# Optimization experiments

Measured on AMD Instinct MI355X. Metric: run time of the kernel, lower is better.

The kernel has to match this reference:

```python
import jax, jax.numpy as jnp
import numpy as np

D_MODEL = 2048
D_INNER = 4096      # expand * d_model
HEADDIM = 64
NHEADS = 64         # d_inner // headdim
D_STATE = 128
NGROUPS = 1
D_CONV = 4
CHUNK = 128
EPS = 1e-5
BATCH = 2
SEQLEN = 4096
D_CONV_CH = D_INNER + 2 * NGROUPS * D_STATE            # 4352
D_IN_PROJ = 2 * D_INNER + 2 * NGROUPS * D_STATE + NHEADS  # 8512


def setup_inputs() -> dict:
    ks = jax.random.split(jax.random.key(0), 9)
    u = jax.random.normal(ks[0], (BATCH, SEQLEN, D_MODEL), jnp.float32)
    W_in = jax.random.normal(ks[1], (D_MODEL, D_IN_PROJ), jnp.float32) * 0.02
    conv_w = jax.random.normal(ks[2], (D_CONV_CH, D_CONV), jnp.float32) * 0.2
    conv_b = jax.random.normal(ks[3], (D_CONV_CH,), jnp.float32) * 0.02
    dt_bias = jax.random.normal(ks[4], (NHEADS,), jnp.float32) * 0.1
    A_log = jax.random.normal(ks[5], (NHEADS,), jnp.float32) * 0.1
    D = jnp.ones((NHEADS,), jnp.float32)
    norm_w = jnp.ones((D_INNER,), jnp.float32)
    W_out = jax.random.normal(ks[8], (D_INNER, D_MODEL), jnp.float32) * 0.02
    return dict(u=u, W_in=W_in, conv_w=conv_w, conv_b=conv_b, dt_bias=dt_bias,
                A_log=A_log, D=D, norm_w=norm_w, W_out=W_out)


def _mamba2_forward(u, W_in, conv_w, conv_b, dt_bias, A_log, D, norm_w, W_out):
    b, L, _ = u.shape
    zxbcdt = u @ W_in                                       # (b, L, 8512)
    z = zxbcdt[..., :D_INNER]
    xBC = zxbcdt[..., D_INNER:D_INNER + D_CONV_CH]
    dt = zxbcdt[..., D_INNER + D_CONV_CH:]                  # (b, L, h)

    # causal depthwise conv1d (padding = d_conv-1, truncated to L) + SiLU
    padded = jnp.pad(xBC, ((0, 0), (D_CONV - 1, 0), (0, 0)))
    xBC_conv = conv_b + sum(padded[:, k:k + L, :] * conv_w[:, k] for k in range(D_CONV))
    xBC_act = jax.nn.silu(xBC_conv)

    x = xBC_act[..., :D_INNER].reshape(b, L, NHEADS, HEADDIM)
    Bm = xBC_act[..., D_INNER:D_INNER + NGROUPS * D_STATE].reshape(b, L, NGROUPS, D_STATE)
    Cm = xBC_act[..., D_INNER + NGROUPS * D_STATE:].reshape(b, L, NGROUPS, D_STATE)
    rep = NHEADS // NGROUPS
    Bh = jnp.repeat(Bm, rep, axis=2)                        # (b, L, h, n)
    Ch = jnp.repeat(Cm, rep, axis=2)

    A = -jnp.exp(A_log)                                     # (h,), negative
    dtf = jax.nn.softplus(dt + dt_bias)                     # (b, L, h)

    # ---- chunked SSD (structured state-space duality) scan ----
    nc = L // CHUNK
    xc = x.reshape(b, nc, CHUNK, NHEADS, HEADDIM)
    Bc = Bh.reshape(b, nc, CHUNK, NHEADS, D_STATE)
    Cc = Ch.reshape(b, nc, CHUNK, NHEADS, D_STATE)
    dtc = dtf.reshape(b, nc, CHUNK, NHEADS)
    cum = jnp.cumsum(dtc * A, axis=2)                       # (b, nc, cs, h), decreasing

    # intra-chunk causal decay matrix L_ij = exp(cum_i - cum_j), i >= j
    idx = jnp.arange(CHUNK)
    mask = (idx[:, None] >= idx[None, :])[None, None, :, :, None]
    seg = cum[:, :, :, None, :] - cum[:, :, None, :, :]     # (b, nc, i, j, h)
    decay = jnp.exp(jnp.where(mask, seg, -jnp.inf))
    CB = jnp.einsum('bcihn,bcjhn->bcijh', Cc, Bc)
    Y_diag = jnp.einsum('bcijh,bcjh,bcjhp->bcihp', CB * decay, dtc, xc)

    # per-chunk final states: sum_j exp(cum_last - cum_j) * dt_j * B_j (x) x_j
    decay_last = jnp.exp(cum[:, :, -1:, :] - cum)           # (b, nc, cs, h)
    states = jnp.einsum('bclh,bclhn,bclhp->bchpn', decay_last * dtc, Bc, xc)

    # inter-chunk recurrence: carry_{c+1} = exp(sum dA_c) * carry_c + states_c
    Atot = jnp.exp(cum[:, :, -1, :])                        # (b, nc, h)
    def step(carry, inp):
        a, s = inp
        return a[..., None, None] * carry + s, carry
    init = jnp.zeros((b, NHEADS, HEADDIM, D_STATE), jnp.float32)
    _, prev = jax.lax.scan(step, init, (jnp.moveaxis(Atot, 1, 0), jnp.moveaxis(states, 1, 0)))
    prev = jnp.moveaxis(prev, 0, 1)                         # (b, nc, h, p, n) state entering each chunk

    Y_off = jnp.einsum('bclhn,bclh,bchpn->bclhp', Cc, jnp.exp(cum), prev)

    y = (Y_diag + Y_off).reshape(b, L, NHEADS, HEADDIM) + D[:, None] * x
    y = y.reshape(b, L, D_INNER)

    # gated RMSNorm: rmsnorm(y * silu(z)) * norm_w
    t = y * jax.nn.silu(z)
    t = t * jax.lax.rsqrt(jnp.mean(t * t, axis=-1, keepdims=True) + EPS) * norm_w
    return t @ W_out


def reference(u, W_in, conv_w, conv_b, dt_bias, A_log, D, norm_w, W_out):
    return _mamba2_forward(u, W_in, conv_w, conv_b, dt_bias, A_log, D, norm_w, W_out)
```

## Files before the change

### kernel.cpp

```cpp
#include <hip/hip_runtime.h>

#define BATCH 2
#define SEQLEN 4096
#define DM 2048
#define DIP 8512
#define DIPP 8576
#define DI 4096
#define DCC 4352
#define NH 64
#define HD 64
#define DSZ 128
#define CHK 128
#define NC 32
#define NBL (BATCH*SEQLEN)
#define LDP 136

typedef __attribute__((ext_vector_type(4))) float f32x4;
typedef __attribute__((ext_vector_type(8))) __bf16 bf16x8;
typedef __attribute__((ext_vector_type(8))) unsigned short us8;
typedef __attribute__((ext_vector_type(4))) unsigned short us4;

__device__ inline float bf2f(unsigned short u){ union{unsigned int i; float f;} v; v.i=((unsigned)u)<<16; return v.f; }
__device__ inline unsigned short f2bf(float f){ union{float f; unsigned int i;} v; v.f=f; unsigned r=(v.i + 0x7FFFu + ((v.i>>16)&1u))>>16; return (unsigned short)r; }

#define GLOAD_LDS16(gp, lp) __builtin_amdgcn_global_load_lds( \
    (const __attribute__((address_space(1))) void*)(gp), \
    (__attribute__((address_space(3))) void*)(lp), 16, 0, 0)

__global__ void beacon_kernel(float* __restrict__ out, float v)
{
    if (blockIdx.x == 0 && threadIdx.x == 0) out[0] = v;
}

__global__ void cast_bf16_kernel(const float* __restrict__ src, unsigned short* __restrict__ dst, size_t n)
{
    size_t stride = (size_t)gridDim.x * blockDim.x * 8;
    for (size_t i = ((size_t)blockIdx.x*blockDim.x + threadIdx.x)*8; i < n; i += stride) {
        float4 a = *(const float4*)&src[i];
        float4 b = *(const float4*)&src[i+4];
        us8 o;
        o[0]=f2bf(a.x); o[1]=f2bf(a.y); o[2]=f2bf(a.z); o[3]=f2bf(a.w);
        o[4]=f2bf(b.x); o[5]=f2bf(b.y); o[6]=f2bf(b.z); o[7]=f2bf(b.w);
        *(us8*)&dst[i] = o;
    }
}

__global__ __launch_bounds__(256) void transpose_cast_kernel(
    const float* __restrict__ in, unsigned short* __restrict__ out, int R, int C)
{
    __shared__ float tile[32][33];
    const int c0 = blockIdx.x*32, r0 = blockIdx.y*32;
    const int tx = threadIdx.x & 31, ty = threadIdx.x >> 5;
    #pragma unroll
    for (int i = 0; i < 4; i++) {
        const int r = r0 + ty + i*8;
        const int c = c0 + tx;
        tile[ty+i*8][tx] = (c < C) ? in[(size_t)r*C + c] : 0.f;
    }
    __syncthreads();
    #pragma unroll
    for (int i = 0; i < 4; i++) {
        const int cc = c0 + ty + i*8;
        const int rr = r0 + tx;
        out[(size_t)cc*R + rr] = f2bf(tile[tx][ty+i*8]);
    }
}

template<int EPI>
__global__ __launch_bounds__(512, 1) void gemm256(
    const unsigned short* __restrict__ A, const unsigned short* __restrict__ Bt,
    float* __restrict__ C, int K, int ldc, int Nmax,
    unsigned short* __restrict__ zbf, unsigned short* __restrict__ xbcbf,
    float* __restrict__ dtf, const float* __restrict__ dt_bias)
{
    __shared__ unsigned short L[65536];
    const int m0 = blockIdx.x * 256;
    const int n0 = blockIdx.y * 256;
    const int tid = threadIdx.x;
    const int lane = tid & 63;
    const int wid  = tid >> 6;
    const int wm = wid >> 2, wn = wid & 3;
    const int lr  = lane & 15;
    const int lkg = (lane >> 4) * 8;
    const int srow = (wid << 4) + (lane >> 3);
    const int scol = ((lane & 7) ^ (lane >> 3)) << 3;
    const int cs0 = lkg ^ ((lr & 7) << 3);
    const int cs1 = cs0 ^ 32;
    const int nt = K >> 6;

    f32x4 acc[8][4];
    #pragma unroll
    for (int i=0;i<8;i++)
        #pragma unroll
        for (int j=0;j<4;j++) acc[i][j] = f32x4{0.f,0.f,0.f,0.f};

    auto stA = [&](int buf, int t, int h) {
        const unsigned short* g = A + (size_t)(m0 + h*128 + srow)*K + t*64 + scol;
        GLOAD_LDS16(g,               &L[buf*32768 + h*8192 + wid*1024]);
        GLOAD_LDS16(g + (size_t)8*K, &L[buf*32768 + h*8192 + wid*1024 + 512]);
    };
    auto stB = [&](int buf, int t, int h) {
        const int rr = n0 + h*128 + srow;
        const int r0 = (rr     > Nmax) ? Nmax : rr;
        const int r1 = (rr + 8 > Nmax) ? Nmax : rr + 8;
        GLOAD_LDS16(Bt + (size_t)r0*K + t*64 + scol, &L[buf*32768 + 16384 + h*8192 + wid*1024]);
        GLOAD_LDS16(Bt + (size_t)r1*K + t*64 + scol, &L[buf*32768 + 16384 + h*8192 + wid*1024 + 512]);
    };
    auto rdA = [&](int buf, int mq, int s, int ks) {
        const int rl = mq*32 + s*16 + lr;
        return *(const bf16x8*)&L[buf*32768 + wm*8192 + rl*64 + (ks ? cs1 : cs0)];
    };
    auto rdB = [&](int buf, int nf, int ks) {
        const int rl = (wn & 1)*64 + nf*16 + lr;
        return *(const bf16x8*)&L[buf*32768 + 16384 + (wn >> 1)*8192 + rl*64 + (ks ? cs1 : cs0)];
    };

    bf16x8 bfr[4][2];
#define PH(BUF, MQ, LOADB, ...) do { \
    bf16x8 af[2][2]; \
    af[0][0]=rdA(BUF,MQ,0,0); af[0][1]=rdA(BUF,MQ,0,1); \
    af[1][0]=rdA(BUF,MQ,1,0); af[1][1]=rdA(BUF,MQ,1,1); \
    if (LOADB) { \
        _Pragma("unroll") \
        for (int nf=0;nf<4;nf++){ bfr[nf][0]=rdB(BUF,nf,0); bfr[nf][1]=rdB(BUF,nf,1);} } \
    __VA_ARGS__; \
    if (LOADB) asm volatile("s_waitcnt lgkmcnt(8)" ::: "memory"); \
    asm volatile("s_barrier" ::: "memory"); \
    __builtin_amdgcn_s_setprio(1); \
    _Pragma("unroll") \
    for (int s=0;s<2;s++) { \
        _Pragma("unroll") \
        for (int nf=0;nf<4;nf++) { \
            acc[(MQ)*2+s][nf] = __builtin_amdgcn_mfma_f32_16x16x32_bf16(af[s][0], bfr[nf][0], acc[(MQ)*2+s][nf], 0,0,0); \
            acc[(MQ)*2+s][nf] = __builtin_amdgcn_mfma_f32_16x16x32_bf16(af[s][1], bfr[nf][1], acc[(MQ)*2+s][nf], 0,0,0); } } \
    __builtin_amdgcn_s_setprio(0); \
    asm volatile("s_barrier" ::: "memory"); \
} while(0)

    stA(0, 0, 0); stA(0, 0, 1); stB(0, 0, 0); stB(0, 0, 1);
    stB(1, 1, 0); stB(1, 1, 1);
    asm volatile("s_waitcnt vmcnt(4)" ::: "memory");
    asm volatile("s_barrier" ::: "memory");

    #pragma unroll 1
    for (int t = 0; t < nt; t += 2) {
        const int tp2 = (t + 2 < nt) ? t + 2 : nt - 1;
        const int tp3 = (t + 3 < nt) ? t + 3 : nt - 1;
        PH(0, 0, true,  stA(1, t+1, 0));
        PH(0, 1, false, stA(1, t+1, 1); stB(0, tp2, 0));
        PH(0, 2, false, stB(0, tp2, 1));
        PH(0, 3, false, asm volatile("s_waitcnt vmcnt(4)" ::: "memory"));
        PH(1, 0, true,  stA(0, tp2, 0));
        PH(1, 1, false, stA(0, tp2, 1); stB(1, tp3, 0));
        PH(1, 2, false, stB(1, tp3, 1));
        PH(1, 3, false, asm volatile("s_waitcnt vmcnt(4)" ::: "memory"));
    }
#undef PH

    const int cr = (lane >> 4) * 4;
    const int cc = lane & 15;
    #pragma unroll
    for (int i=0;i<8;i++) {
        #pragma unroll
        for (int j=0;j<4;j++) {
            const int row = m0 + wm*128 + i*16 + cr;
            const int col = n0 + wn*64 + j*16 + cc;
            #pragma unroll
            for (int r=0;r<4;r++) {
                const float val = acc[i][j][r];
                const int rr = row + r;
                if (EPI == 0) {
                    C[(size_t)rr*ldc + col] = val;
                } else {
                    if (col < DI) {
                        zbf[(size_t)rr*DI + col] = f2bf(val);
                    } else if (col < DI + DCC) {
                        xbcbf[(size_t)rr*DCC + (col - DI)] = f2bf(val);
                    } else if (col < DI + DCC + NH) {
                        const int hh = col - (DI + DCC);
                        const float x = val + dt_bias[hh];
                        dtf[(size_t)rr*NH + hh] = (x > 20.f) ? x : log1pf(__expf(x));
                    }
                }
            }
        }
    }
}

__global__ __launch_bounds__(256) void conv_x_kernel(
    const unsigned short* __restrict__ xbc,
    const float* __restrict__ cw, const float* __restrict__ cb,
    unsigned short* __restrict__ xT,
    unsigned short* __restrict__ bcbf)
{
    __shared__ float raw[67][68];
    __shared__ unsigned short ot[64][72];
    const int lt = blockIdx.x;
    const int h  = blockIdx.y;
    const int b  = lt >> 6;
    const int l0 = (lt & 63) * 64;
    const int t = threadIdx.x;

    if (h >= 64) {
        const int g4 = h - 64;
        #pragma unroll
        for (int j = 0; j < 2; j++) {
            const int u = t + j*256;
            const int l = u >> 3, pg = (u & 7)*8;
            const int ch0 = DI + g4*64 + pg;
            const int row = b*SEQLEN + l0 + l;
            float a[8];
            #pragma unroll
            for (int e=0;e<8;e++) a[e] = cb[ch0+e];
            #pragma unroll
            for (int k = 0; k < 4; k++) {
                if (l0 + l + k >= 3) {
                    us8 v = *(const us8*)&xbc[(size_t)(row + k - 3)*DCC + ch0];
                    #pragma unroll
                    for (int e=0;e<8;e++) a[e] += bf2f(v[e]) * cw[(ch0+e)*4 + k];
                }
            }
            us8 o;
            #pragma unroll
            for (int e=0;e<8;e++){ const float s = a[e]/(1.f+__expf(-a[e])); o[e]=f2bf(s); }
            *(us8*)&bcbf[(size_t)row*256 + g4*64 + pg] = o;
        }
        return;
    }

    for (int i = t; i < 536; i += 256) {
        const int li = i >> 3, cg = (i & 7) * 8;
        const int l = l0 - 3 + li;
        us8 v;
        #pragma unroll
        for (int e = 0; e < 8; e++) v[e] = 0;
        if (l >= 0) v = *(const us8*)&xbc[(size_t)(b*SEQLEN + l)*DCC + h*64 + cg];
        #pragma unroll
        for (int e = 0; e < 8; e++) raw[li][cg+e] = bf2f(v[e]);
    }
    __syncthreads();
    #pragma unroll
    for (int j = 0; j < 16; j++) {
        const int i = t + j*256;
        const int l = i >> 6, p = i & 63;
        const int ch = h*64 + p;
        float a = cb[ch];
        #pragma unroll
        for (int k = 0; k < 4; k++) a += raw[l + k][p] * cw[ch*4 + k];
        a = a / (1.f + __expf(-a));
        ot[l][p] = f2bf(a);
    }
    __syncthreads();
    for (int i = t; i < 512; i += 256) {
        const int p = i >> 3, lg = (i & 7) * 8;
        us8 o;
        #pragma unroll
        for (int e = 0; e < 8; e++) o[e] = ot[lg + e][p];
        *(us8*)&xT[(size_t)((b*NH + h)*HD + p)*SEQLEN + l0 + lg] = o;
    }
}

__global__ void cum_kernel(const float* __restrict__ dtf, const float* __restrict__ A_log,
                           float* __restrict__ cum)
{
    const int idx = blockIdx.x*blockDim.x + threadIdx.x;
    if (idx >= BATCH*NC*NH) return;
    const int h = idx & 63;
    const int bc = idx >> 6;
    const float A = -__expf(A_log[h]);
    float c = 0.f;
    const float* src = dtf + (size_t)bc*CHK*NH + h;
    float* dst = cum + (size_t)bc*CHK*NH + h;
    for (int i = 0; i < CHK; i++) { c += src[i*NH]*A; dst[i*NH] = c; }
}

__global__ __launch_bounds__(256, 3) void ssm_passS(
    const unsigned short* __restrict__ bcbf,
    const unsigned short* __restrict__ xT,
    const float* __restrict__ cumg,
    const float* __restrict__ dtfg,
    unsigned short* __restrict__ states)
{
    __shared__ unsigned short BT[128*LDP];
    __shared__ float w_s[128];

    const int blk = blockIdx.x;
    const int h = blk & 63;
    const int bc = blk >> 6;
    const int r0 = bc * CHK;
    const int t = threadIdx.x;
    const int lane = t & 63;
    const int wid = t >> 6;

    if (t < 128) {
        const float cl = cumg[(size_t)(r0+127)*NH + h];
        const float ci = cumg[(size_t)(r0+t)*NH + h];
        const float dt = dtfg[(size_t)(r0+t)*NH + h];
        w_s[t] = __expf(cl - ci) * dt;
    }
    for (int i = t; i < 2048; i += 256) {
        const int l = i >> 4, cg = (i & 15)*8;
        us8 v = *(const us8*)(bcbf + (size_t)(r0+l)*256 + cg);
        #pragma unroll
        for (int e = 0; e < 8; e++) BT[(cg+e)*LDP + l] = v[e];
    }
    __syncthreads();

    const int lr = lane & 15;
    const int lkg = (lane >> 4)*8;
    const int wr = wid >> 1, wc = wid & 1;
    const int b = bc >> 5;
    const int li = (bc & 31) * CHK;
    const unsigned short* xb = xT + (size_t)((b*NH + h)*HD)*SEQLEN + li;

    f32x4 acc[2][4];
    #pragma unroll
    for (int i=0;i<2;i++)
        #pragma unroll
        for (int j=0;j<4;j++) acc[i][j] = f32x4{0.f,0.f,0.f,0.f};
    #pragma unroll
    for (int k = 0; k < 4; k++) {
        bf16x8 a[2], bfr[4];
        #pragma unroll
        for (int i=0;i<2;i++) {
            us8 xv = *(const us8*)(xb + (size_t)(wr*32 + i*16 + lr)*SEQLEN + k*32 + lkg);
            us8 aw;
            #pragma unroll
            for (int e=0;e<8;e++) aw[e] = f2bf(bf2f(xv[e]) * w_s[k*32 + lkg + e]);
            a[i] = __builtin_bit_cast(bf16x8, aw);
        }
        #pragma unroll
        for (int j=0;j<4;j++) bfr[j] = *(const bf16x8*)&BT[(wc*64 + j*16 + lr)*LDP + k*32 + lkg];
        #pragma unroll
        for (int i=0;i<2;i++)
            #pragma unroll
            for (int j=0;j<4;j++)
                acc[i][j] = __builtin_amdgcn_mfma_f32_16x16x32_bf16(a[i], bfr[j], acc[i][j], 0,0,0);
    }
    unsigned short* sb = states + (size_t)blk * (HD*DSZ);
    const int cr = (lane >> 4)*4, cc = lane & 15;
    #pragma unroll
    for (int i=0;i<2;i++) {
        #pragma unroll
        for (int j=0;j<4;j++) {
            const int nn = wc*64 + j*16 + cc;
            #pragma unroll
            for (int r=0;r<4;r++) {
                const int pp = wr*32 + i*16 + cr + r;
                sb[pp*DSZ + nn] = f2bf(acc[i][j][r]);
            }
        }
    }
}

__global__ void scan_kernel(unsigned short* __restrict__ states, const float* __restrict__ cumg)
{
    const int idx = blockIdx.x*256 + threadIdx.x;
    const int n = idx & 127;
    const int p = (idx >> 7) & 63;
    const int h = (idx >> 13) & 63;
    const int b = idx >> 19;
    float carry = 0.f;
    for (int c = 0; c < NC; c++) {
        const size_t off = ((size_t)((b*NC + c)*NH + h))*(HD*DSZ) + p*DSZ + n;
        const float s = bf2f(states[off]);
        states[off] = f2bf(carry);
        const float atot = __expf(cumg[(size_t)((b*NC+c)*CHK + 127)*NH + h]);
        carry = atot*carry + s;
    }
}

__global__ __launch_bounds__(256, 3) void ssm_passY(
    const unsigned short* __restrict__ bcbf,
    const unsigned short* __restrict__ xT,
    const unsigned short* __restrict__ statesg,
    const float* __restrict__ cumg,
    const float* __restrict__ dtfg,
    const float* __restrict__ Dg,
    unsigned short* __restrict__ y)
{
    __shared__ unsigned short P1[128*LDP];
    __shared__ float cum_s[128], dtc_s[128];

    const int blk = blockIdx.x;
    const int h = blk & 63;
    const int bc = blk >> 6;
    const int r0 = bc * CHK;
    const int t = threadIdx.x;
    const int lane = t & 63;
    const int wid = t >> 6;

    if (t < 128) {
        cum_s[t] = cumg[(size_t)(r0+t)*NH + h];
        dtc_s[t] = dtfg[(size_t)(r0+t)*NH + h];
    }
    for (int i = t; i < 2048; i += 256) {
        const int l = i >> 4, cg = (i & 15)*8;
        *(us8*)&P1[l*LDP + cg] = *(const us8*)(bcbf + (size_t)(r0+l)*256 + 128 + cg);
    }
    __syncthreads();

    const int lr = lane & 15;
    const int lkg = (lane >> 4)*8;
    const int wr = wid >> 1, wc = wid & 1;
    const int b = bc >> 5;
    const int li = (bc & 31) * CHK;
    const unsigned short* xb = xT + (size_t)((b*NH + h)*HD)*SEQLEN + li;
    const unsigned short* sb = statesg + (size_t)blk * (HD*DSZ);
    const unsigned short* bb = bcbf + (size_t)r0*256;

    f32x4 acc1[4][4], acc2[4][2];
    #pragma unroll
    for (int i=0;i<4;i++) {
        #pragma unroll
        for (int j=0;j<4;j++) acc1[i][j] = f32x4{0.f,0.f,0.f,0.f};
        #pragma unroll
        for (int j=0;j<2;j++) acc2[i][j] = f32x4{0.f,0.f,0.f,0.f};
    }
    #pragma unroll
    for (int k = 0; k < 4; k++) {
        bf16x8 a[4], bfr[4], pv[2];
        #pragma unroll
        for (int i=0;i<4;i++) a[i] = *(const bf16x8*)&P1[(wr*64 + i*16 + lr)*LDP + k*32 + lkg];
        #pragma unroll
        for (int j=0;j<4;j++) bfr[j] = *(const bf16x8*)(bb + (size_t)(wc*64 + j*16 + lr)*256 + k*32 + lkg);
        #pragma unroll
        for (int j=0;j<2;j++) pv[j] = *(const bf16x8*)(sb + (size_t)(wc*32 + j*16 + lr)*DSZ + k*32 + lkg);
        #pragma unroll
        for (int i=0;i<4;i++) {
            #pragma unroll
            for (int j=0;j<4;j++)
                acc1[i][j] = __builtin_amdgcn_mfma_f32_16x16x32_bf16(a[i], bfr[j], acc1[i][j], 0,0,0);
            #pragma unroll
            for (int j=0;j<2;j++)
                acc2[i][j] = __builtin_amdgcn_mfma_f32_16x16x32_bf16(a[i], pv[j], acc2[i][j], 0,0,0);
        }
    }
    __syncthreads();
    const int cr = (lane >> 4)*4, cc = lane & 15;
    #pragma unroll
    for (int i=0;i<4;i++) {
        #pragma unroll
        for (int j=0;j<4;j++) {
            const int jj = wc*64 + j*16 + cc;
            #pragma unroll
            for (int r=0;r<4;r++) {
                const int ii = wr*64 + i*16 + cr + r;
                float v = 0.f;
                if (jj <= ii) v = acc1[i][j][r] * __expf(cum_s[ii] - cum_s[jj]) * dtc_s[jj];
                P1[ii*LDP + jj] = f2bf(v);
            }
        }
    }
    __syncthreads();
    #pragma unroll
    for (int i=0;i<4;i++) {
        #pragma unroll
        for (int r=0;r<4;r++) {
            const int ii = wr*64 + i*16 + cr + r;
            const float sc = __expf(cum_s[ii]);
            #pragma unroll
            for (int j=0;j<2;j++) acc2[i][j][r] *= sc;
        }
    }
    #pragma unroll
    for (int k = 0; k < 4; k++) {
        bf16x8 a[4], x2[2];
        #pragma unroll
        for (int i=0;i<4;i++) a[i] = *(const bf16x8*)&P1[(wr*64 + i*16 + lr)*LDP + k*32 + lkg];
        #pragma unroll
        for (int j=0;j<2;j++) x2[j] = *(const bf16x8*)(xb + (size_t)(wc*32 + j*16 + lr)*SEQLEN + k*32 + lkg);
        #pragma unroll
        for (int i=0;i<4;i++)
            #pragma unroll
            for (int j=0;j<2;j++)
                acc2[i][j] = __builtin_amdgcn_mfma_f32_16x16x32_bf16(a[i], x2[j], acc2[i][j], 0,0,0);
    }
    const float Dv = Dg[h];
    #pragma unroll
    for (int i=0;i<4;i++) {
        #pragma unroll
        for (int j=0;j<2;j++) {
            const int pp = wc*32 + j*16 + cc;
            #pragma unroll
            for (int r=0;r<4;r++) {
                const int ii = wr*64 + i*16 + cr + r;
                const float xv = bf2f(xb[(size_t)pp*SEQLEN + ii]);
                y[(size_t)(r0+ii)*DI + h*64 + pp] = f2bf(acc2[i][j][r] + Dv * xv);
            }
        }
    }
}

__global__ __launch_bounds__(256) void gate_rms_kernel(
    const unsigned short* __restrict__ y, const unsigned short* __restrict__ z,
    const float* __restrict__ nw, unsigned short* __restrict__ tbf)
{
    const int row = blockIdx.x;
    const int t = threadIdx.x;
    const int lane = t & 63, wid = t >> 6;
    float tv[16];
    float ss = 0.f;
    #pragma unroll
    for (int i = 0; i < 2; i++) {
        const int c = (i*256 + t)*8;
        const us8 yv = *(const us8*)&y[(size_t)row*DI + c];
        const us8 zv = *(const us8*)&z[(size_t)row*DI + c];
        #pragma unroll
        for (int e = 0; e < 8; e++) {
            const float fy = bf2f(yv[e]);
            const float fz = bf2f(zv[e]);
            const float v = fy * (fz / (1.f + __expf(-fz)));
            tv[i*8+e] = v;
            ss += v*v;
        }
    }
    #pragma unroll
    for (int o = 1; o < 64; o <<= 1) ss += __shfl_xor(ss, o, 64);
    __shared__ float red[4];
    if (lane == 0) red[wid] = ss;
    __syncthreads();
    const float rms = rsqrtf((red[0]+red[1]+red[2]+red[3]) * (1.f/DI) + 1e-5f);
    #pragma unroll
    for (int i = 0; i < 2; i++) {
        const int c = (i*256 + t)*8;
        us8 o;
        #pragma unroll
        for (int e = 0; e < 8; e += 4) {
            const float4 wv = *(const float4*)&nw[c + e];
            o[e+0]=f2bf(tv[i*8+e+0]*rms*wv.x);
            o[e+1]=f2bf(tv[i*8+e+1]*rms*wv.y);
            o[e+2]=f2bf(tv[i*8+e+2]*rms*wv.z);
            o[e+3]=f2bf(tv[i*8+e+3]*rms*wv.w);
        }
        *(us8*)&tbf[(size_t)row*DI + c] = o;
    }
}

extern "C" void kernel_launch(void* const* d_in, const int* in_sizes, int n_in,
                              void* d_out, int out_size, void* d_ws, size_t ws_size,
                              hipStream_t stream)
{
    const float* u       = (const float*)d_in[0];
    const float* W_in    = (const float*)d_in[1];
    const float* conv_w  = (const float*)d_in[2];
    const float* conv_b  = (const float*)d_in[3];
    const float* dt_bias = (const float*)d_in[4];
    const float* A_log   = (const float*)d_in[5];
    const float* Dp      = (const float*)d_in[6];
    const float* norm_w  = (const float*)d_in[7];
    const float* W_out   = (const float*)d_in[8];
    float* out = (float*)d_out;

    char* ws = (char*)d_ws;
    const size_t OFF_WINT = 33554432;
    const size_t OFF_R2   = 68681728;
    const size_t OFF_R3   = 139984896;
    const size_t OFF_SM   = 207093760;
    const size_t NEED     = OFF_SM + 2097152 + 2097152 + 4194304;
    if (ws_size < NEED) {
        beacon_kernel<<<1, 64, 0, stream>>>(out, 10000.f + (float)(ws_size >> 20));
        return;
    }

    unsigned short* u_bf   = (unsigned short*)(ws);
    unsigned short* winT   = (unsigned short*)(ws + OFF_WINT);
    unsigned short* xTb    = (unsigned short*)(ws);
    unsigned short* t_bf   = (unsigned short*)(ws);
    unsigned short* xbc_bf = (unsigned short*)(ws + OFF_R2);
    unsigned short* y_bf   = (unsigned short*)(ws + OFF_R2);
    unsigned short* states = (unsigned short*)(ws + OFF_R3);
    unsigned short* woutT  = (unsigned short*)(ws + OFF_R3);
    float*          dtf    = (float*)(ws + OFF_SM);
    float*          cum    = (float*)(ws + OFF_SM + 2097152);
    unsigned short* bc_bf  = (unsigned short*)(ws + OFF_SM + 4194304);
    unsigned short* z_bf   = (unsigned short*)d_out;

    cast_bf16_kernel<<<2048, 256, 0, stream>>>(u, u_bf, (size_t)NBL*DM);
    transpose_cast_kernel<<<dim3(DIPP/32, DM/32), 256, 0, stream>>>(W_in, winT, DM, DIP);
    gemm256<1><<<dim3(NBL/256, (DIPP+255)/256), 512, 0, stream>>>(
        u_bf, winT, nullptr, DM, 0, DIPP-1, z_bf, xbc_bf, dtf, dt_bias);
    conv_x_kernel<<<dim3(NBL/64, NH+4), 256, 0, stream>>>(xbc_bf, conv_w, conv_b, xTb, bc_bf);
    cum_kernel<<<64, 64, 0, stream>>>(dtf, A_log, cum);
    ssm_passS<<<BATCH*NC*NH, 256, 0, stream>>>(bc_bf, xTb, cum, dtf, states);
    scan_kernel<<<4096, 256, 0, stream>>>(states, cum);
    ssm_passY<<<BATCH*NC*NH, 256, 0, stream>>>(bc_bf, xTb, states, cum, dtf, Dp, y_bf);
    gate_rms_kernel<<<NBL, 256, 0, stream>>>(y_bf, z_bf, norm_w, t_bf);
    transpose_cast_kernel<<<dim3(DM/32, DI/32), 256, 0, stream>>>(W_out, woutT, DI, DM);
    gemm256<0><<<dim3(NBL/256, DM/256), 512, 0, stream>>>(
        t_bf, woutT, out, DI, DM, DM-1, nullptr, nullptr, nullptr, nullptr);
}
```

Measured before the change: 871.8 us.

## Software-pipeline LDS fragment reads in GEMM and fold D skip into diagonal

The GEMM main loop now double-buffers A and B register fragments, so the LDS reads for the next quarter are issued before the current quarter's MFMAs instead of directly ahead of them. The aim is to hide LDS latency behind MFMA work. The explicit lgkmcnt wait is dropped, leaving ordering to the barriers and compiler-inserted waits. Separately, the SSD chunk kernel adds D to the diagonal of the intra-chunk matrix, which removes the strided per-element x reload in the epilogue. In exchange, D is rounded to bf16 and register pressure goes up.

```diff
diff --git a/kernel.cpp b/kernel.cpp
--- a/kernel.cpp
+++ b/kernel.cpp
@@ -115,47 +115,61 @@
         return *(const bf16x8*)&L[buf*32768 + 16384 + (wn >> 1)*8192 + rl*64 + (ks ? cs1 : cs0)];
     };
 
-    bf16x8 bfr[4][2];
-#define PH(BUF, MQ, LOADB, ...) do { \
-    bf16x8 af[2][2]; \
-    af[0][0]=rdA(BUF,MQ,0,0); af[0][1]=rdA(BUF,MQ,0,1); \
-    af[1][0]=rdA(BUF,MQ,1,0); af[1][1]=rdA(BUF,MQ,1,1); \
-    if (LOADB) { \
-        _Pragma("unroll") \
-        for (int nf=0;nf<4;nf++){ bfr[nf][0]=rdB(BUF,nf,0); bfr[nf][1]=rdB(BUF,nf,1);} } \
-    __VA_ARGS__; \
-    if (LOADB) asm volatile("s_waitcnt lgkmcnt(8)" ::: "memory"); \
-    asm volatile("s_barrier" ::: "memory"); \
+#define BAR asm volatile("s_barrier" ::: "memory")
+#define VM4 asm volatile("s_waitcnt vmcnt(4)" ::: "memory")
+#define RD_A(AF, BUF, MQ) do { \
+    AF[0][0]=rdA(BUF,MQ,0,0); AF[0][1]=rdA(BUF,MQ,0,1); \
+    AF[1][0]=rdA(BUF,MQ,1,0); AF[1][1]=rdA(BUF,MQ,1,1); } while(0)
+#define RD_B(BF, BUF) do { \
+    _Pragma("unroll") \
+    for (int nf=0;nf<4;nf++){ BF[nf][0]=rdB(BUF,nf,0); BF[nf][1]=rdB(BUF,nf,1);} } while(0)
+#define MFMA_Q(MQ, AF, BF) do { \
     __builtin_amdgcn_s_setprio(1); \
     _Pragma("unroll") \
     for (int s=0;s<2;s++) { \
         _Pragma("unroll") \
         for (int nf=0;nf<4;nf++) { \
-            acc[(MQ)*2+s][nf] = __builtin_amdgcn_mfma_f32_16x16x32_bf16(af[s][0], bfr[nf][0], acc[(MQ)*2+s][nf], 0,0,0); \
-            acc[(MQ)*2+s][nf] = __builtin_amdgcn_mfma_f32_16x16x32_bf16(af[s][1], bfr[nf][1], acc[(MQ)*2+s][nf], 0,0,0); } } \
+            acc[(MQ)*2+s][nf] = __builtin_amdgcn_mfma_f32_16x16x32_bf16(AF[s][0], BF[nf][0], acc[(MQ)*2+s][nf], 0,0,0); \
+            acc[(MQ)*2+s][nf] = __builtin_amdgcn_mfma_f32_16x16x32_bf16(AF[s][1], BF[nf][1], acc[(MQ)*2+s][nf], 0,0,0); } } \
     __builtin_amdgcn_s_setprio(0); \
-    asm volatile("s_barrier" ::: "memory"); \
 } while(0)
 
     stA(0, 0, 0); stA(0, 0, 1); stB(0, 0, 0); stB(0, 0, 1);
     stB(1, 1, 0); stB(1, 1, 1);
-    asm volatile("s_waitcnt vmcnt(4)" ::: "memory");
-    asm volatile("s_barrier" ::: "memory");
+    VM4;
+    BAR;
+    bf16x8 afA[2][2], afB[2][2], bfA[4][2], bfB[4][2];
+    RD_A(afA, 0, 0);
+    RD_B(bfA, 0);
 
     #pragma unroll 1
     for (int t = 0; t < nt; t += 2) {
         const int tp2 = (t + 2 < nt) ? t + 2 : nt - 1;
         const int tp3 = (t + 3 < nt) ? t + 3 : nt - 1;
-        PH(0, 0, true,  stA(1, t+1, 0));
-        PH(0, 1, false, stA(1, t+1, 1); stB(0, tp2, 0));
-        PH(0, 2, false, stB(0, tp2, 1));
-        PH(0, 3, false, asm volatile("s_waitcnt vmcnt(4)" ::: "memory"));
-        PH(1, 0, true,  stA(0, tp2, 0));
-        PH(1, 1, false, stA(0, tp2, 1); stB(1, tp3, 0));
-        PH(1, 2, false, stB(1, tp3, 1));
-        PH(1, 3, false, asm volatile("s_waitcnt vmcnt(4)" ::: "memory"));
-    }
-#undef PH
+        RD_A(afB, 0, 1); stA(1, t+1, 0);
+        BAR; MFMA_Q(0, afA, bfA); BAR;
+        RD_A(afA, 0, 2); stA(1, t+1, 1); stB(0, tp2, 0);
+        BAR; MFMA_Q(1, afB, bfA); BAR;
+        RD_A(afB, 0, 3); stB(0, tp2, 1);
+        VM4;
+        BAR; MFMA_Q(2, afA, bfA); BAR;
+        RD_A(afA, 1, 0); RD_B(bfB, 1);
+        BAR; MFMA_Q(3, afB, bfA); BAR;
+        RD_A(afB, 1, 1); stA(0, tp2, 0);
+        BAR; MFMA_Q(0, afA, bfB); BAR;
+        RD_A(afA, 1, 2); stA(0, tp2, 1); stB(1, tp3, 0);
+        BAR; MFMA_Q(1, afB, bfB); BAR;
+        RD_A(afB, 1, 3); stB(1, tp3, 1);
+        VM4;
+        BAR; MFMA_Q(2, afA, bfB); BAR;
+        RD_A(afA, 0, 0); RD_B(bfA, 0);
+        BAR; MFMA_Q(3, afB, bfB); BAR;
+    }
+#undef BAR
+#undef VM4
+#undef RD_A
+#undef RD_B
+#undef MFMA_Q
 
     const int cr = (lane >> 4) * 4;
     const int cc = lane & 15;
@@ -437,6 +451,7 @@
         }
     }
     __syncthreads();
+    const float Dv = Dg[h];
     const int cr = (lane >> 4)*4, cc = lane & 15;
     #pragma unroll
     for (int i=0;i<4;i++) {
@@ -448,6 +463,7 @@
                 const int ii = wr*64 + i*16 + cr + r;
                 float v = 0.f;
                 if (jj <= ii) v = acc1[i][j][r] * __expf(cum_s[ii] - cum_s[jj]) * dtc_s[jj];
+                if (jj == ii) v += Dv;
                 P1[ii*LDP + jj] = f2bf(v);
             }
         }
@@ -476,7 +492,6 @@
             for (int j=0;j<2;j++)
                 acc2[i][j] = __builtin_amdgcn_mfma_f32_16x16x32_bf16(a[i], x2[j], acc2[i][j], 0,0,0);
     }
-    const float Dv = Dg[h];
     #pragma unroll
     for (int i=0;i<4;i++) {
         #pragma unroll
@@ -485,8 +500,7 @@
             #pragma unroll
             for (int r=0;r<4;r++) {
                 const int ii = wr*64 + i*16 + cr + r;
-                const float xv = bf2f(xb[(size_t)pp*SEQLEN + ii]);
-                y[(size_t)(r0+ii)*DI + h*64 + pp] = f2bf(acc2[i][j][r] + Dv * xv);
+                y[(size_t)(r0+ii)*DI + h*64 + pp] = f2bf(acc2[i][j][r]);
             }
         }
     }
```

After: 890.6 us. 2.2% more time.
